# Optimization experiments

Measured on AMD Instinct MI355X. Metric: run time of the kernel, lower is better.

Reference implementation:

```python
import math
import jax, jax.numpy as jnp
import numpy as np

H = 8          # n_heads (params['h'])
TOPK_K = 2     # params['k']
TAU = 25       # moving-average window (params['tau'])


def ma_decomp(x, tau):
    """MADecompositionLayer: edge-pad by tau, centered moving average of width tau."""
    B, L, D = x.shape
    front = jnp.repeat(x[:, :1], tau, axis=1)
    back = jnp.repeat(x[:, -1:], tau, axis=1)
    padded = jnp.concatenate([front, x, back], axis=1)          # (B, L+2tau, D)
    cs = jnp.cumsum(padded, axis=1)
    cs = jnp.concatenate([jnp.zeros_like(cs[:, :1]), cs], axis=1)
    off = tau - (tau - 1) // 2  # start offset of the SAME-padded pool window
    trend = (cs[:, off + tau: off + tau + L] - cs[:, off: off + L]) / tau
    return x - trend, trend     # (seasonality, trend)


def corr_attention(x, Wq, bq, Wk, bk, Wv, bv, Wo, bo):
    """CorrLayer (inference path: per-sample top-k delay aggregation)."""
    B, L, D = x.shape
    dk = D // H
    # projections -> (B, h, d, L)
    q = (x @ Wq + bq).reshape(B, L, H, dk).transpose(0, 2, 3, 1)
    k = (x @ Wk + bk).reshape(B, L, H, dk).transpose(0, 2, 3, 1)
    v = (x @ Wv + bv).reshape(B, L, H, dk).transpose(0, 2, 3, 1)
    # FFT cross-correlation as written in the source:
    # corr = irfft(real = qr*kr, imag = -(qi*ki))
    qf = jnp.fft.rfft(q, axis=-1)
    kf = jnp.fft.rfft(k, axis=-1)
    spec = (qf.real * kf.real) - 1j * (qf.imag * kf.imag)
    corr = jnp.fft.irfft(spec, n=L, axis=-1)                    # (B, h, d, L)
    # top-k delay selection per sample
    top_k = min(int(TOPK_K * math.log(L)), L)
    mean_value = corr.mean(axis=(1, 2))                          # (B, L)
    weights, delay = jax.lax.top_k(mean_value, top_k)            # (B, topk)
    w = jax.nn.softmax(weights, axis=-1)                         # (B, topk)
    # circular-shift gather: values[..., (delay + arange(L)) % L]
    idx = (delay[:, :, None] + jnp.arange(L)[None, None, :]) % L  # (B, topk, L)
    rolled = jnp.take_along_axis(v[:, None], idx[:, :, None, None, :], axis=-1)  # (B, topk, h, d, L)
    agg = jnp.einsum('bt,bthdl->bhdl', w, rolled)                # (B, h, d, L)
    out = agg.transpose(0, 3, 1, 2).reshape(B, L, H * dk)        # (B, L, D)
    return out @ Wo + bo


def setup_inputs() -> dict:
    key = jax.random.key(0)
    ks = jax.random.split(key, 8)
    B, L, D, DFF = 8, 2048, 512, 2048
    s = 0.02
    return {
        'x':  jax.random.normal(ks[0], (B, L, D), jnp.float32),
        'Wq': jax.random.normal(ks[1], (D, D), jnp.float32) * s,
        'bq': jnp.zeros((D,), jnp.float32),
        'Wk': jax.random.normal(ks[2], (D, D), jnp.float32) * s,
        'bk': jnp.zeros((D,), jnp.float32),
        'Wv': jax.random.normal(ks[3], (D, D), jnp.float32) * s,
        'bv': jnp.zeros((D,), jnp.float32),
        'Wo': jax.random.normal(ks[4], (D, D), jnp.float32) * s,
        'bo': jnp.zeros((D,), jnp.float32),
        'W1': jax.random.normal(ks[5], (D, DFF), jnp.float32) * s,
        'W2': jax.random.normal(ks[6], (DFF, D), jnp.float32) * s,
    }


def reference(x, Wq, bq, Wk, bk, Wv, bv, Wo, bo, W1, W2):
    # Autoformer encoder layer: attn + residual, decomp, FFN, decomp
    attn_out = corr_attention(x, Wq, bq, Wk, bk, Wv, bv, Wo, bo)
    xr = x + attn_out                       # dropout_rate = 0.0
    s1, _ = ma_decomp(xr, TAU)
    y = jax.nn.relu(s1 @ W1) @ W2           # FFN (bias-free, as in Autoformer conv1d)
    s2, _ = ma_decomp(s1 + y, TAU)
    return s2
```

## Files before the change

### kernel.cpp

```cpp
#include <hip/hip_runtime.h>
#include <math.h>

namespace {
constexpr int kB = 8;
constexpr int kL = 2048;
constexpr int kD = 512;
constexpr int kTopk = 15;
constexpr int kLMask = 2047;
}

typedef unsigned short u16;
using f32x4 = __attribute__((ext_vector_type(4))) float;
using bf16x8 = __attribute__((ext_vector_type(8))) __bf16;

__device__ __forceinline__ u16 f2b(float f) {
  unsigned u = __float_as_uint(f);
  unsigned r = (u + 0x7fffu + ((u >> 16) & 1u)) >> 16;
  return (u16)r;
}
__device__ __forceinline__ float b2f(u16 u) {
  return __uint_as_float(((unsigned)u) << 16);
}

typedef __attribute__((address_space(3))) unsigned int lds_u32;
typedef __attribute__((address_space(1))) const unsigned int glb_u32;
__device__ __forceinline__ void gl2lds16(const void* g, void* l) {
  __builtin_amdgcn_global_load_lds((glb_u32*)g, (lds_u32*)l, 16, 0, 0);
}

template <int SPLIT, int RELU, int OUTF, int OUTB, int RES>
__global__ __launch_bounds__(256)
void mfma_gemm(const u16* __restrict__ A, const u16* __restrict__ Bt,
               const float* __restrict__ bias, const float* __restrict__ ResF,
               const u16* __restrict__ ResB, float* __restrict__ outF,
               u16* __restrict__ outB, int N, int K, int lda, int ldb, int nbn) {
  __shared__ u16 As[128 * 64];
  __shared__ u16 Bs[128 * 64];
  int lin = blockIdx.x;
  int split = 0;
  if (SPLIT) { split = lin >> 9; lin &= 511; }
  const int xcd = lin & 7;
  const int s = lin >> 3;
  const int q = s / nbn;
  const int bm = xcd * 16 + q;
  const int bn = s - q * nbn;
  const int tid = threadIdx.x;
  const int wave = tid >> 6;
  const int lane = tid & 63;
  const int ln = lane & 15;
  const int quad = lane >> 4;
  const int wm = (wave >> 1) * 64;
  const int wn = (wave & 1) * 64;
  const int srow = tid >> 3;
  const int scol = (tid & 7) * 8;

  const size_t koff = (size_t)split * K;
  const u16* Ab = A + koff + (size_t)(bm * 128) * lda + scol;
  const u16* Bb = Bt + koff + (size_t)(bn * 128) * ldb + scol;
  char* ldsA = (char*)As + wave * 1024;
  char* ldsB = (char*)Bs + wave * 1024;

  f32x4 acc[4][4];
#pragma unroll
  for (int i = 0; i < 4; ++i)
#pragma unroll
    for (int j = 0; j < 4; ++j) acc[i][j] = (f32x4){0.f, 0.f, 0.f, 0.f};

  for (int k0 = 0; k0 < K; k0 += 64) {
#pragma unroll
    for (int c = 0; c < 4; ++c) {
      gl2lds16(Ab + (size_t)(srow + 32 * c) * lda + k0, ldsA + c * 4096);
      gl2lds16(Bb + (size_t)(srow + 32 * c) * ldb + k0, ldsB + c * 4096);
    }
    __syncthreads();
#pragma unroll
    for (int kk = 0; kk < 2; ++kk) {
      bf16x8 af[4], bfr[4];
#pragma unroll
      for (int i = 0; i < 4; ++i)
        af[i] = *(const bf16x8*)(As + (wm + i * 16 + ln) * 64 + kk * 32 + quad * 8);
#pragma unroll
      for (int j = 0; j < 4; ++j)
        bfr[j] = *(const bf16x8*)(Bs + (wn + j * 16 + ln) * 64 + kk * 32 + quad * 8);
#pragma unroll
      for (int i = 0; i < 4; ++i)
#pragma unroll
        for (int j = 0; j < 4; ++j)
          acc[i][j] = __builtin_amdgcn_mfma_f32_16x16x32_bf16(bfr[j], af[i], acc[i][j], 0, 0, 0);
    }
    __syncthreads();
  }

  const size_t cbase = (size_t)split * ((size_t)16384 * N);
  const bool res2 = (RES == 2) && (!SPLIT || split == 0);
#pragma unroll
  for (int i = 0; i < 4; ++i) {
    const int row = bm * 128 + wm + i * 16 + ln;
#pragma unroll
    for (int j = 0; j < 4; ++j) {
      const int col = bn * 128 + wn + j * 16 + quad * 4;
      f32x4 v = acc[i][j];
      if (bias) {
        float4 bv = *(const float4*)(bias + col);
        v[0] += bv.x; v[1] += bv.y; v[2] += bv.z; v[3] += bv.w;
      }
      if (RES == 1) {
        float4 rv = *(const float4*)(ResF + (size_t)row * N + col);
        v[0] += rv.x; v[1] += rv.y; v[2] += rv.z; v[3] += rv.w;
      }
      if (RES == 2) {
        if (res2) {
          ushort4 rv = *(const ushort4*)(ResB + (size_t)row * N + col);
          v[0] += b2f(rv.x); v[1] += b2f(rv.y); v[2] += b2f(rv.z); v[3] += b2f(rv.w);
        }
      }
      if (RELU) {
#pragma unroll
        for (int r = 0; r < 4; ++r) v[r] = fmaxf(v[r], 0.f);
      }
      if (OUTF) {
        float4 o = {v[0], v[1], v[2], v[3]};
        *(float4*)(outF + cbase + (size_t)row * N + col) = o;
      }
      if (OUTB) {
        ushort4 o = {f2b(v[0]), f2b(v[1]), f2b(v[2]), f2b(v[3])};
        *(ushort4*)(outB + cbase + (size_t)row * N + col) = o;
      }
    }
  }
}

#define RDA(BUF, I, KK) \
  (*(const bf16x8*)&sm[BUF][0][arow + (I) * 1024 + ((KK) ? cx1 : cx0)])
#define RDB(BUF, J, KK) \
  (*(const bf16x8*)&sm[BUF][1][brow + (J) * 1024 + ((KK) ? cx1 : cx0)])
#define STAGE_A(BUF, Q, T) \
  gl2lds16(Ab + (size_t)(Q) * 64 * lda + (size_t)(T) * 64, \
           &sm[BUF][0][((Q) * 64 + wave * 8) * 64])
#define STAGE_B(BUF, Q, T) \
  gl2lds16(Bb + (size_t)(Q) * 64 * ldb + (size_t)(T) * 64, \
           &sm[BUF][1][((Q) * 64 + wave * 8) * 64])
#define MFMA1(i, j, kk, areg) \
  acc[i][j] = __builtin_amdgcn_mfma_f32_16x16x32_bf16(bf[j][kk], areg, acc[i][j], 0, 0, 0)
#define PHASE_MFMA(I0, A0k0, A0k1, A1k0, A1k1)                                 \
  MFMA1(I0, 0, 0, A0k0); MFMA1(I0, 1, 0, A0k0);                                \
  MFMA1(I0, 2, 0, A0k0); MFMA1(I0, 3, 0, A0k0);                                \
  MFMA1((I0) + 1, 0, 0, A1k0); MFMA1((I0) + 1, 1, 0, A1k0);                    \
  MFMA1((I0) + 1, 2, 0, A1k0); MFMA1((I0) + 1, 3, 0, A1k0);                    \
  MFMA1(I0, 0, 1, A0k1); MFMA1(I0, 1, 1, A0k1);                                \
  MFMA1(I0, 2, 1, A0k1); MFMA1(I0, 3, 1, A0k1);                                \
  MFMA1((I0) + 1, 0, 1, A1k1); MFMA1((I0) + 1, 1, 1, A1k1);                    \
  MFMA1((I0) + 1, 2, 1, A1k1); MFMA1((I0) + 1, 3, 1, A1k1)

#define GTILE(CUR, T)                                                          \
  {                                                                            \
    constexpr int NXT = (CUR) ^ 1;                                             \
    const bool hn = (T) + 1 < NT;                                              \
    const int tn = (T) + 1;                                                    \
    bf16x8 bf[4][2];                                                           \
    {                                                             \
      bf16x8 a00 = RDA(CUR, 0, 0), a01 = RDA(CUR, 0, 1);                       \
      bf16x8 a10 = RDA(CUR, 1, 0), a11 = RDA(CUR, 1, 1);                       \
      bf[0][0] = RDB(CUR, 0, 0); bf[0][1] = RDB(CUR, 0, 1);                    \
      bf[1][0] = RDB(CUR, 1, 0); bf[1][1] = RDB(CUR, 1, 1);                    \
      bf[2][0] = RDB(CUR, 2, 0); bf[2][1] = RDB(CUR, 2, 1);                    \
      bf[3][0] = RDB(CUR, 3, 0); bf[3][1] = RDB(CUR, 3, 1);                    \
      if (hn) { STAGE_B(NXT, 0, tn); STAGE_B(NXT, 1, tn); }                    \
      asm volatile("s_barrier" ::: "memory");                                  \
      __builtin_amdgcn_s_setprio(1);                                           \
      PHASE_MFMA(0, a00, a01, a10, a11);                                       \
      __builtin_amdgcn_s_setprio(0);                                           \
      asm volatile("s_barrier" ::: "memory");                                  \
    }                                                                          \
    {                                                             \
      bf16x8 a00 = RDA(CUR, 2, 0), a01 = RDA(CUR, 2, 1);                       \
      bf16x8 a10 = RDA(CUR, 3, 0), a11 = RDA(CUR, 3, 1);                       \
      if (hn) { STAGE_B(NXT, 2, tn); STAGE_B(NXT, 3, tn); }                    \
      asm volatile("s_barrier" ::: "memory");                                  \
      __builtin_amdgcn_s_setprio(1);                                           \
      PHASE_MFMA(2, a00, a01, a10, a11);                                       \
      __builtin_amdgcn_s_setprio(0);                                           \
      if (hn) { asm volatile("s_waitcnt vmcnt(4)" ::: "memory"); }             \
      else    { asm volatile("s_waitcnt vmcnt(0)" ::: "memory"); }             \
      asm volatile("s_barrier" ::: "memory");                                  \
    }                                                                          \
    {                                                             \
      bf16x8 a00 = RDA(CUR, 4, 0), a01 = RDA(CUR, 4, 1);                       \
      bf16x8 a10 = RDA(CUR, 5, 0), a11 = RDA(CUR, 5, 1);                       \
      if (hn) { STAGE_A(NXT, 0, tn); STAGE_A(NXT, 2, tn); }                    \
      asm volatile("s_barrier" ::: "memory");                                  \
      __builtin_amdgcn_s_setprio(1);                                           \
      PHASE_MFMA(4, a00, a01, a10, a11);                                       \
      __builtin_amdgcn_s_setprio(0);                                           \
      asm volatile("s_barrier" ::: "memory");                                  \
    }                                                                          \
    {                                                             \
      bf16x8 a00 = RDA(CUR, 6, 0), a01 = RDA(CUR, 6, 1);                       \
      bf16x8 a10 = RDA(CUR, 7, 0), a11 = RDA(CUR, 7, 1);                       \
      if (hn) { STAGE_A(NXT, 1, tn); STAGE_A(NXT, 3, tn); }                    \
      asm volatile("s_barrier" ::: "memory");                                  \
      __builtin_amdgcn_s_setprio(1);                                           \
      PHASE_MFMA(6, a00, a01, a10, a11);                                       \
      __builtin_amdgcn_s_setprio(0);                                           \
      if (hn) { asm volatile("s_waitcnt vmcnt(2)" ::: "memory"); }             \
      asm volatile("s_barrier" ::: "memory");                                  \
    }                                                                          \
  }

template <int SPLITK, int RELU, int HAS_BIAS, int OUTF, int RES>
__global__ __launch_bounds__(512, 2)
void gemm256(const u16* __restrict__ A, const u16* __restrict__ Bt,
             const float* __restrict__ bias, const u16* __restrict__ ResB,
             u16* __restrict__ outB, float* __restrict__ outF,
             int N, int K, int lda, int ldb, int nbn) {
  __shared__ u16 sm[2][2][256 * 64];
  const int lin = blockIdx.x;
  int bm, bn, split = 0;
  if (SPLITK) {
    const int xcd = lin & 7;
    const int s = lin >> 3;
    bm = xcd * 8 + (s & 7);
    bn = (s >> 3) & 1;
    split = s >> 4;
  } else {
    const int chunk = (int)gridDim.x >> 3;
    const int gid = (lin & 7) * chunk + (lin >> 3);
    bm = gid / nbn;
    bn = gid - bm * nbn;
  }

  const int tid = threadIdx.x;
  const int wave = tid >> 6;
  const int lane = tid & 63;
  const int ln = lane & 15;
  const int quad = lane >> 4;
  const int wm = (wave >> 2) * 128;
  const int wn = (wave & 3) * 64;

  const int srow = tid >> 3;
  const int schunk = (tid & 7) ^ (srow & 7);

  const size_t koff = (size_t)split * K;
  const u16* Ab = A + koff + (size_t)(bm * 256 + srow) * lda + schunk * 8;
  const u16* Bb = Bt + koff + (size_t)(bn * 256 + srow) * ldb + schunk * 8;

  const int cx0 = ((quad) ^ (ln & 7)) * 8;
  const int cx1 = ((4 | quad) ^ (ln & 7)) * 8;
  const int arow = (wm + ln) * 64;
  const int brow = (wn + ln) * 64;

  const int NT = K >> 6;

  f32x4 acc[8][4];
#pragma unroll
  for (int i = 0; i < 8; ++i)
#pragma unroll
    for (int j = 0; j < 4; ++j) acc[i][j] = (f32x4){0.f, 0.f, 0.f, 0.f};

  STAGE_B(0, 0, 0); STAGE_B(0, 1, 0); STAGE_B(0, 2, 0); STAGE_B(0, 3, 0);
  STAGE_A(0, 0, 0); STAGE_A(0, 2, 0); STAGE_A(0, 1, 0); STAGE_A(0, 3, 0);
  asm volatile("s_waitcnt vmcnt(2)" ::: "memory");
  asm volatile("s_barrier" ::: "memory");

  for (int t = 0; t < NT; t += 2) {
    GTILE(0, t);
    GTILE(1, t + 1);
  }

  const int col0 = bn * 256 + wn + quad * 4;
  const size_t cbase = (size_t)split * ((size_t)16384 * N);
  const int wmh = wm >> 1;

#pragma unroll
  for (int chunk = 0; chunk < 2; ++chunk) {
    if (chunk) {
      asm volatile("s_waitcnt lgkmcnt(0)" ::: "memory");
      asm volatile("s_barrier" ::: "memory");
    }
#pragma unroll
    for (int i2 = 0; i2 < 4; ++i2) {
      const int i = chunk * 4 + i2;
      const int lr = wmh + i2 * 16 + ln;
      const size_t row = (size_t)(bm * 256 + wm + i * 16 + ln);
#pragma unroll
      for (int j = 0; j < 4; ++j) {
        const int col = col0 + j * 16;
        const int ct = wn + j * 16 + quad * 4;
        f32x4 v = acc[i][j];
        if (HAS_BIAS) {
          float4 bv = *(const float4*)(bias + col);
          v[0] += bv.x; v[1] += bv.y; v[2] += bv.z; v[3] += bv.w;
        }
        if (RES == 2) {
          if (split == 0) {
            ushort4 rv = *(const ushort4*)(ResB + row * N + col);
            v[0] += b2f(rv.x); v[1] += b2f(rv.y); v[2] += b2f(rv.z); v[3] += b2f(rv.w);
          }
        }
        if (RELU) {
          v[0] = fmaxf(v[0], 0.f); v[1] = fmaxf(v[1], 0.f);
          v[2] = fmaxf(v[2], 0.f); v[3] = fmaxf(v[3], 0.f);
        }
        if (OUTF) {
          float* scrF = (float*)&sm[0][0][0];
          const int off = (lr * 1024 + ct * 4) ^ ((lr & 7) << 4);
          *(f32x4*)((char*)scrF + off) = v;
        } else {
          u16* scr = (u16*)&sm[0][0][0];
          ushort4 o = {f2b(v[0]), f2b(v[1]), f2b(v[2]), f2b(v[3])};
          const int off = (lr * 512 + ct * 2) ^ ((lr & 7) << 4);
          *(ushort4*)((char*)scr + off) = o;
        }
      }
    }
    asm volatile("s_waitcnt lgkmcnt(0)" ::: "memory");
    asm volatile("s_barrier" ::: "memory");
    if (OUTF) {
      const float* scrF = (const float*)&sm[0][0][0];
#pragma unroll
      for (int it = 0; it < 16; ++it) {
        const int idx = it * 512 + tid;
        const int r = idx >> 6;
        const int u = idx & 63;
        const int src = r * 1024 + ((u ^ (r & 7)) << 4);
        f32x4 d = *(const f32x4*)((const char*)scrF + src);
        const size_t grow = (size_t)(bm * 256 + ((r >> 6) << 7) + chunk * 64 + (r & 63));
        *((f32x4*)(outF + cbase + grow * N + bn * 256) + u) = d;
      }
    } else {
      const u16* scr = (const u16*)&sm[0][0][0];
#pragma unroll
      for (int it = 0; it < 8; ++it) {
        const int idx = it * 512 + tid;
        const int r = idx >> 5;
        const int u = idx & 31;
        const int src = r * 512 + ((u ^ (r & 7)) << 4);
        f32x4 d = *(const f32x4*)((const char*)scr + src);
        const size_t grow = (size_t)(bm * 256 + ((r >> 6) << 7) + chunk * 64 + (r & 63));
        *(f32x4*)((char*)(outB + grow * N + bn * 256) + u * 16) = d;
      }
    }
  }
}

#undef RDA
#undef RDB
#undef STAGE_A
#undef STAGE_B
#undef MFMA1
#undef PHASE_MFMA
#undef GTILE

__global__ __launch_bounds__(256)
void prep_kernel(const float* __restrict__ x,
                 const float* __restrict__ Wq, const float* __restrict__ Wk,
                 const float* __restrict__ Wv, const float* __restrict__ Wo,
                 const float* __restrict__ W1, const float* __restrict__ W2,
                 const float* __restrict__ bq, const float* __restrict__ bk,
                 const float* __restrict__ bv,
                 u16* __restrict__ xb, u16* __restrict__ Wqkvt,
                 u16* __restrict__ W1t, u16* __restrict__ W2t,
                 float* __restrict__ bqkv) {
  __shared__ float tsh[32][33];
  const int blk = blockIdx.x;
  const int tid = threadIdx.x;
  if (blk < 8192) {
    const int i = (blk * 256 + tid) * 4;
    float4 v = *(const float4*)(x + i);
    ushort4 o = {f2b(v.x), f2b(v.y), f2b(v.z), f2b(v.w)};
    *(ushort4*)(xb + i) = o;
  } else if (blk < 9216) {
    const int rem = blk - 8192;
    const int z = rem >> 8;
    const int by = (rem >> 4) & 15;
    const int bx = rem & 15;
    const float* W = z == 0 ? Wq : z == 1 ? Wk : z == 2 ? Wv : Wo;
    u16* Wt = Wqkvt + (size_t)z * 512 * 512;
    const int k0 = by * 32, n0 = bx * 32;
    const int tx = tid & 31, ty = tid >> 5;
    for (int r = ty; r < 32; r += 8)
      tsh[r][tx] = W[(size_t)(k0 + r) * 512 + n0 + tx];
    __syncthreads();
    for (int r = ty; r < 32; r += 8)
      Wt[(size_t)(n0 + r) * 512 + k0 + tx] = f2b(tsh[tx][r]);
  } else if (blk < 10240) {
    const int rem = blk - 9216;
    const int bx = rem & 63;
    const int by = rem >> 6;
    const int k0 = by * 32, n0 = bx * 32;
    const int tx = tid & 31, ty = tid >> 5;
    for (int r = ty; r < 32; r += 8)
      tsh[r][tx] = W1[(size_t)(k0 + r) * 2048 + n0 + tx];
    __syncthreads();
    for (int r = ty; r < 32; r += 8)
      W1t[(size_t)(n0 + r) * 512 + k0 + tx] = f2b(tsh[tx][r]);
  } else if (blk < 11264) {
    const int rem = blk - 10240;
    const int bx = rem & 15;
    const int by = rem >> 4;
    const int k0 = by * 32, n0 = bx * 32;
    const int tx = tid & 31, ty = tid >> 5;
    for (int r = ty; r < 32; r += 8)
      tsh[r][tx] = W2[(size_t)(k0 + r) * 512 + n0 + tx];
    __syncthreads();
    for (int r = ty; r < 32; r += 8)
      W2t[(size_t)(n0 + r) * 2048 + k0 + tx] = f2b(tsh[tx][r]);
  } else {
    const int i = (blk - 11264) * 256 + tid;
    const float* s = i < 512 ? bq : (i < 1024 ? bk : bv);
    bqkv[i] = s[i & 511];
  }
}

__global__ __launch_bounds__(256)
void fft_corr(const u16* __restrict__ qkv, float* __restrict__ pA,
              float* __restrict__ pB) {
  __shared__ u16 stq[4 * 2048];
  __shared__ u16 stk[4 * 2048];
  __shared__ float re[2048];
  __shared__ float im[2048];
  const int blk = blockIdx.x;
  const int b = blk & 7;
  const int g = blk >> 3;
  const int t = threadIdx.x;
  const float PI = 3.14159265358979323846f;

  const u16* qb = qkv + (size_t)b * kL * 1536 + g * 4;
#pragma unroll
  for (int p = 0; p < 8; ++p) {
    const int row = p * 256 + t;
    *(ushort4*)&stq[row * 4] = *(const ushort4*)(qb + (size_t)row * 1536);
    *(ushort4*)&stk[row * 4] = *(const ushort4*)(qb + (size_t)row * 1536 + 512);
  }

  const int r = t & 31;
  float cA[4], sA[4], cB[2], sB[2], cC, sC;
  float cD[4], sD[4], cE[2], sE[2], cF, sF;
#pragma unroll
  for (int j = 0; j < 4; ++j)
    __sincosf(PI * (float)(t + 256 * j) * (1.f / 1024.f), &sA[j], &cA[j]);
#pragma unroll
  for (int j = 0; j < 2; ++j)
    __sincosf(PI * (float)(t + 256 * j) * (1.f / 512.f), &sB[j], &cB[j]);
  __sincosf(PI * (float)t * (1.f / 256.f), &sC, &cC);
#pragma unroll
  for (int j = 0; j < 4; ++j)
    __sincosf(PI * (float)(r + 32 * j) * (1.f / 128.f), &sD[j], &cD[j]);
#pragma unroll
  for (int j = 0; j < 2; ++j)
    __sincosf(PI * (float)(r + 32 * j) * (1.f / 64.f), &sE[j], &cE[j]);
  __sincosf(PI * (float)r * (1.f / 32.f), &sF, &cF);
  float sgn[5], cS[5], sS[5];
#pragma unroll
  for (int k = 0; k < 5; ++k) {
    const int m = 16 >> k;
    const bool hi = (t & m) != 0;
    float sv, cv;
    __sincosf(PI * (float)(t & (m - 1)) / (float)m, &sv, &cv);
    sgn[k] = hi ? -1.f : 1.f;
    cS[k] = hi ? cv : 1.f;
    sS[k] = hi ? sv : 0.f;
  }

  float accA[8], accB[8];
#pragma unroll
  for (int i = 0; i < 8; ++i) { accA[i] = 0.f; accB[i] = 0.f; }

  const int base2 = (t >> 5) * 256 + r;

#define BFLY(X, Y, CV, SV)                                              \
  { const float dr_ = er[X] - er[Y], di_ = ei[X] - ei[Y];               \
    er[X] += er[Y]; ei[X] += ei[Y];                                     \
    er[Y] = dr_ * (CV) + di_ * (SV); ei[Y] = di_ * (CV) - dr_ * (SV); }

#pragma unroll
  for (int c = 0; c < 4; ++c) {
    __syncthreads();
    float er[8], ei[8];
#pragma unroll
    for (int j = 0; j < 8; ++j) {
      er[j] = b2f(stq[(t + 256 * j) * 4 + c]);
      ei[j] = b2f(stk[(t + 256 * j) * 4 + c]);
    }
    BFLY(0, 4, cA[0], sA[0]); BFLY(1, 5, cA[1], sA[1]);
    BFLY(2, 6, cA[2], sA[2]); BFLY(3, 7, cA[3], sA[3]);
    BFLY(0, 2, cB[0], sB[0]); BFLY(1, 3, cB[1], sB[1]);
    BFLY(4, 6, cB[0], sB[0]); BFLY(5, 7, cB[1], sB[1]);
    BFLY(0, 1, cC, sC); BFLY(2, 3, cC, sC);
    BFLY(4, 5, cC, sC); BFLY(6, 7, cC, sC);
#pragma unroll
    for (int j = 0; j < 8; ++j) {
      re[t + 256 * j] = er[j];
      im[t + 256 * j] = ei[j];
    }
    __syncthreads();
#pragma unroll
    for (int j = 0; j < 8; ++j) {
      er[j] = re[base2 + 32 * j];
      ei[j] = im[base2 + 32 * j];
    }
    BFLY(0, 4, cD[0], sD[0]); BFLY(1, 5, cD[1], sD[1]);
    BFLY(2, 6, cD[2], sD[2]); BFLY(3, 7, cD[3], sD[3]);
    BFLY(0, 2, cE[0], sE[0]); BFLY(1, 3, cE[1], sE[1]);
    BFLY(4, 6, cE[0], sE[0]); BFLY(5, 7, cE[1], sE[1]);
    BFLY(0, 1, cF, sF); BFLY(2, 3, cF, sF);
    BFLY(4, 5, cF, sF); BFLY(6, 7, cF, sF);
#pragma unroll
    for (int k = 0; k < 5; ++k) {
      const int m = 16 >> k;
#pragma unroll
      for (int j = 0; j < 8; ++j) {
        const float otr = __shfl_xor(er[j], m, 64);
        const float oti = __shfl_xor(ei[j], m, 64);
        const float sr = otr + sgn[k] * er[j];
        const float si = oti + sgn[k] * ei[j];
        er[j] = sr * cS[k] + si * sS[k];
        ei[j] = si * cS[k] - sr * sS[k];
      }
    }
    __syncthreads();
#pragma unroll
    for (int j = 0; j < 8; ++j) {
      re[base2 + 32 * j] = er[j];
      im[base2 + 32 * j] = ei[j];
    }
    __syncthreads();
#pragma unroll
    for (int i = 0; i < 8; ++i) {
      const int pos = i * 256 + t;
      const int f = __brev((unsigned)pos) >> 21;
      if (f <= 1024) {
        const int fm = (2048 - f) & 2047;
        const int pm = __brev((unsigned)fm) >> 21;
        const float zr = re[pos], zi = im[pos];
        const float mr = re[pm], mi = im[pm];
        const float ReQ = 0.5f * (zr + mr);
        const float ImQ = 0.5f * (zi - mi);
        const float ReK = 0.5f * (zi + mi);
        const float ImK = 0.5f * (mr - zr);
        accA[i] += ReQ * ReK;
        accB[i] += ImQ * ImK;
      }
    }
  }
#undef BFLY

  float* pAb = pA + (size_t)blk * 1025;
  float* pBb = pB + (size_t)blk * 1025;
#pragma unroll
  for (int i = 0; i < 8; ++i) {
    const int pos = i * 256 + t;
    const int f = __brev((unsigned)pos) >> 21;
    if (f <= 1024) { pAb[f] = accA[i]; pBb[f] = accB[i]; }
  }
}

__global__ __launch_bounds__(256)
void reduceAB(const float* __restrict__ pA, const float* __restrict__ pB,
              float* __restrict__ Asp, float* __restrict__ Bsp) {
  const int b = blockIdx.x;
  const int f = blockIdx.y * 256 + threadIdx.x;
  if (f > 1024) return;
  float sa = 0.f, sb = 0.f;
  for (int g = 0; g < 128; ++g) {
    const size_t idx = (size_t)((g << 3) | b) * 1025 + f;
    sa += pA[idx];
    sb += pB[idx];
  }
  Asp[b * 1025 + f] = sa;
  Bsp[b * 1025 + f] = sb;
}

__global__ __launch_bounds__(256)
void ifft_topk(const float* __restrict__ Asp, const float* __restrict__ Bsp,
               float* __restrict__ wts, int* __restrict__ dly) {
  __shared__ float re[2048];
  __shared__ float im[2048];
  __shared__ float twc[2047];
  __shared__ float tws[2047];
  __shared__ float rv[256];
  __shared__ int ri[256];
  __shared__ float topv[kTopk];
  __shared__ int topi[kTopk];
  const int b = blockIdx.x;
  const int t = threadIdx.x;
  for (int e = t; e < 2047; e += 256) {
    const int s = 31 - __clz(e + 1);
    const int m = 1 << s;
    const int j = e + 1 - m;
    float sv, cv;
    __sincosf((float)j * 3.14159265358979323846f / (float)m, &sv, &cv);
    twc[e] = cv;
    tws[e] = sv;
  }
#pragma unroll
  for (int i = 0; i < 8; ++i) {
    const int f = i * 256 + t;
    float Xr, Xi;
    if (f <= 1024) {
      Xr = Asp[b * 1025 + f];
      Xi = (f == 0 || f == 1024) ? 0.f : -Bsp[b * 1025 + f];
    } else {
      const int gg = 2048 - f;
      Xr = Asp[b * 1025 + gg];
      Xi = Bsp[b * 1025 + gg];
    }
    const int pos = __brev((unsigned)f) >> 21;
    re[pos] = Xr;
    im[pos] = Xi;
  }
  for (int s = 0; s <= 10; ++s) {
    __syncthreads();
    const int m = 1 << s;
    for (int p = 0; p < 4; ++p) {
      const int id = p * 256 + t;
      const int j = id & (m - 1);
      const int i0 = ((id >> s) << (s + 1)) + j;
      const int i1 = i0 + m;
      const int kk = (m - 1) + j;
      const float cv = twc[kk], sv = tws[kk];
      const float br = re[i1], bi = im[i1];
      const float tr = br * cv - bi * sv;
      const float ti = bi * cv + br * sv;
      const float ar = re[i0], ai = im[i0];
      re[i0] = ar + tr;
      im[i0] = ai + ti;
      re[i1] = ar - tr;
      im[i1] = ai - ti;
    }
  }
  __syncthreads();
#pragma unroll
  for (int i = 0; i < 8; ++i) {
    const int n = i * 256 + t;
    im[n] = re[n] * (1.0f / (2048.0f * 512.0f));
  }
  __syncthreads();
  for (int round = 0; round < kTopk; ++round) {
    float bv = -INFINITY;
    int bi = 0x7fffffff;
#pragma unroll
    for (int i = 0; i < 8; ++i) {
      const int n = i * 256 + t;
      const float v = im[n];
      if (v > bv || (v == bv && n < bi)) { bv = v; bi = n; }
    }
    rv[t] = bv;
    ri[t] = bi;
    __syncthreads();
    for (int s = 128; s > 0; s >>= 1) {
      if (t < s) {
        const float v2 = rv[t + s];
        const int i2 = ri[t + s];
        if (v2 > rv[t] || (v2 == rv[t] && i2 < ri[t])) { rv[t] = v2; ri[t] = i2; }
      }
      __syncthreads();
    }
    if (t == 0) {
      topv[round] = rv[0];
      topi[round] = ri[0];
      im[ri[0]] = -INFINITY;
    }
    __syncthreads();
  }
  if (t == 0) {
    const float m = topv[0];
    float sum = 0.f;
    float e[kTopk];
    for (int i = 0; i < kTopk; ++i) { e[i] = expf(topv[i] - m); sum += e[i]; }
    for (int i = 0; i < kTopk; ++i) {
      wts[b * 16 + i] = e[i] / sum;
      dly[b * 16 + i] = topi[i];
    }
  }
}

__global__ __launch_bounds__(256)
void agg_kernel(const u16* __restrict__ qkv, const float* __restrict__ wts,
                const int* __restrict__ dly, u16* __restrict__ out) {
  __shared__ float w[16];
  __shared__ int dl[16];
  const int lin = blockIdx.x;
  const int b = lin & 7;
  if (threadIdx.x < kTopk) {
    w[threadIdx.x] = wts[b * 16 + threadIdx.x];
    dl[threadIdx.x] = dly[b * 16 + threadIdx.x];
  }
  __syncthreads();
  const int l = (lin >> 3) * 4 + (threadIdx.x >> 6);
  const int co = (threadIdx.x & 63) * 8;
  const u16* vb = qkv + (size_t)b * kL * 1536 + 1024 + co;
  float a[8] = {0.f, 0.f, 0.f, 0.f, 0.f, 0.f, 0.f, 0.f};
  for (int t = 0; t < kTopk; ++t) {
    const int row = (l + dl[t]) & kLMask;
    float4 rv = *(const float4*)(vb + (size_t)row * 1536);
    const u16* p = (const u16*)&rv;
    const float wt = w[t];
#pragma unroll
    for (int e = 0; e < 8; ++e) a[e] += wt * b2f(p[e]);
  }
  u16 ob[8];
#pragma unroll
  for (int e = 0; e < 8; ++e) ob[e] = f2b(a[e]);
  *(float4*)(out + ((size_t)b * kL + l) * kD + co) = *(const float4*)ob;
}

__global__ __launch_bounds__(256)
void decomp_b2b(const u16* __restrict__ X, u16* __restrict__ OB) {
  const int c = blockIdx.x * 256 + threadIdx.x;
  const int b = blockIdx.y;
  const int l0 = blockIdx.z * 64;
  const u16* base = X + (size_t)b * kL * kD + c;
  float sum = 0.f;
#pragma unroll
  for (int m = -12; m <= 12; ++m) {
    int lm = l0 + m;
    lm = lm < 0 ? 0 : (lm > kL - 1 ? kL - 1 : lm);
    sum += b2f(base[(size_t)lm * kD]);
  }
#pragma unroll 4
  for (int l = l0; l < l0 + 64; ++l) {
    const float val = b2f(base[(size_t)l * kD]);
    OB[((size_t)b * kL + l) * kD + c] = f2b(val - sum * (1.0f / 25.0f));
    const int la = l + 13 > kL - 1 ? kL - 1 : l + 13;
    const int lr = l - 12 < 0 ? 0 : l - 12;
    sum += b2f(base[(size_t)la * kD]) - b2f(base[(size_t)lr * kD]);
  }
}

__global__ __launch_bounds__(256)
void decomp_ff2(const float* __restrict__ X1, const float* __restrict__ X2,
                float* __restrict__ OF) {
  const int c = blockIdx.x * 256 + threadIdx.x;
  const int b = blockIdx.y;
  const int l0 = blockIdx.z * 64;
  const size_t off = (size_t)b * kL * kD + c;
  const float* b1 = X1 + off;
  const float* b2 = X2 + off;
  float sum = 0.f;
#pragma unroll
  for (int m = -12; m <= 12; ++m) {
    int lm = l0 + m;
    lm = lm < 0 ? 0 : (lm > kL - 1 ? kL - 1 : lm);
    sum += b1[(size_t)lm * kD] + b2[(size_t)lm * kD];
  }
#pragma unroll 4
  for (int l = l0; l < l0 + 64; ++l) {
    const float val = b1[(size_t)l * kD] + b2[(size_t)l * kD];
    OF[((size_t)b * kL + l) * kD + c] = val - sum * (1.0f / 25.0f);
    const int la = l + 13 > kL - 1 ? kL - 1 : l + 13;
    const int lr = l - 12 < 0 ? 0 : l - 12;
    sum += b1[(size_t)la * kD] + b2[(size_t)la * kD]
         - b1[(size_t)lr * kD] - b2[(size_t)lr * kD];
  }
}

extern "C" void kernel_launch(void* const* d_in, const int* in_sizes, int n_in,
                              void* d_out, int out_size, void* d_ws, size_t ws_size,
                              hipStream_t stream) {
  const float* x  = (const float*)d_in[0];
  const float* Wq = (const float*)d_in[1];
  const float* bq = (const float*)d_in[2];
  const float* Wk = (const float*)d_in[3];
  const float* bk = (const float*)d_in[4];
  const float* Wv = (const float*)d_in[5];
  const float* bv = (const float*)d_in[6];
  const float* Wo = (const float*)d_in[7];
  const float* bo = (const float*)d_in[8];
  const float* W1 = (const float*)d_in[9];
  const float* W2 = (const float*)d_in[10];
  float* out = (float*)d_out;

  const size_t MiB = 1u << 20;
  const size_t NBLD = (size_t)kB * kL * kD;
  char* base = (char*)d_ws;
  u16*   qkvb  = (u16*)(base);
  u16*   xb    = (u16*)(base + 48 * MiB);
  u16*   aggb  = xb;
  u16*   xrb   = (u16*)(base + 64 * MiB);
  u16*   s1b   = (u16*)(base + 80 * MiB);
  u16*   midb  = (u16*)(base + 96 * MiB);
  float* s2p   = (float*)(base);
  u16*   Wqkvt = (u16*)(base + 160 * MiB);
  u16*   Wot   = Wqkvt + 3 * 512 * 512;
  u16*   W1t   = (u16*)(base + 162 * MiB);
  u16*   W2t   = (u16*)(base + 164 * MiB);
  float* bqkv  = (float*)(base + 166 * MiB);
  float* Asp   = bqkv + 2048;
  float* Bsp   = Asp + kB * 1025;
  float* wtsf  = Bsp + kB * 1025;
  int*   dlyi  = (int*)(wtsf + kB * 16);
  float* pA    = (float*)(base + 167 * MiB);
  float* pB    = (float*)(base + 172 * MiB);

  const dim3 blk(256);
  const dim3 blk512(512);

  prep_kernel<<<dim3(11270), blk, 0, stream>>>(
      x, Wq, Wk, Wv, Wo, W1, W2, bq, bk, bv, xb, Wqkvt, W1t, W2t, bqkv);

  gemm256<0, 0, 1, 0, 0><<<dim3(384), blk512, 0, stream>>>(
      xb, Wqkvt, bqkv, nullptr, qkvb, nullptr, 1536, 512, 512, 512, 6);

  fft_corr<<<dim3(1024), blk, 0, stream>>>(qkvb, pA, pB);
  reduceAB<<<dim3(8, 5), blk, 0, stream>>>(pA, pB, Asp, Bsp);
  ifft_topk<<<dim3(8), blk, 0, stream>>>(Asp, Bsp, wtsf, dlyi);

  agg_kernel<<<dim3(4096), blk, 0, stream>>>(qkvb, wtsf, dlyi, aggb);
  mfma_gemm<0, 0, 0, 1, 1><<<dim3(512), blk, 0, stream>>>(
      aggb, Wot, bo, x, nullptr, nullptr, xrb, 512, 512, 512, 512, 4);

  decomp_b2b<<<dim3(2, 8, 32), blk, 0, stream>>>(xrb, s1b);

  gemm256<0, 1, 0, 0, 0><<<dim3(512), blk512, 0, stream>>>(
      s1b, W1t, nullptr, nullptr, midb, nullptr, 2048, 512, 512, 512, 8);

  gemm256<1, 0, 0, 1, 2><<<dim3(256), blk512, 0, stream>>>(
      midb, W2t, nullptr, s1b, nullptr, s2p, 512, 1024, 2048, 2048, 2);

  decomp_ff2<<<dim3(2, 8, 32), blk, 0, stream>>>(s2p, s2p + NBLD, out);
}
```

Baseline: 403.5 us.

## Replace 256-tile pipelined GEMM with unified swizzled 128-tile GEMM

Removes the 256x256 double-buffered, phase-scheduled gemm256 kernel and the old mfma_gemm, replacing all four GEMMs with a single 128x128 tile kernel. The new kernel uses XOR-swizzled LDS staging and an LDS-staged coalesced epilogue, with no double buffering. Grids grow to 4x more blocks of 256 threads. This trades operand reuse and load/compute overlap for more parallelism and a simpler single-buffer loop, which risks more global traffic and exposed load latency on the larger GEMMs.

Measured after the change: 426.7 us. +5.8%, slower.

```diff
diff --git a/kernel.cpp b/kernel.cpp
--- a/kernel.cpp
+++ b/kernel.cpp
@@ -28,22 +28,25 @@
   __builtin_amdgcn_global_load_lds((glb_u32*)g, (lds_u32*)l, 16, 0, 0);
 }
 
-template <int SPLIT, int RELU, int OUTF, int OUTB, int RES>
-__global__ __launch_bounds__(256)
-void mfma_gemm(const u16* __restrict__ A, const u16* __restrict__ Bt,
-               const float* __restrict__ bias, const float* __restrict__ ResF,
-               const u16* __restrict__ ResB, float* __restrict__ outF,
-               u16* __restrict__ outB, int N, int K, int lda, int ldb, int nbn) {
-  __shared__ u16 As[128 * 64];
-  __shared__ u16 Bs[128 * 64];
+template <int SPLITK, int RELU, int HAS_BIAS, int OUTF, int RES>
+__global__ __launch_bounds__(256)
+void gemm128(const u16* __restrict__ A, const u16* __restrict__ Bt,
+             const float* __restrict__ bias, const float* __restrict__ ResF,
+             const u16* __restrict__ ResB, u16* __restrict__ outB,
+             float* __restrict__ outF, int N, int K, int lda, int ldb, int nbn) {
+  __shared__ __align__(16) u16 smu[2][128 * 64];
+  u16* As = &smu[0][0];
+  u16* Bs = &smu[1][0];
+
   int lin = blockIdx.x;
   int split = 0;
-  if (SPLIT) { split = lin >> 9; lin &= 511; }
-  const int xcd = lin & 7;
-  const int s = lin >> 3;
-  const int q = s / nbn;
-  const int bm = xcd * 16 + q;
-  const int bn = s - q * nbn;
+  const int g2 = SPLITK ? ((int)gridDim.x >> 1) : (int)gridDim.x;
+  if (SPLITK && lin >= g2) { split = 1; lin -= g2; }
+  const int chunkx = g2 >> 3;
+  const int gid = (lin & 7) * chunkx + (lin >> 3);
+  const int bm = gid / nbn;
+  const int bn = gid - bm * nbn;
+
   const int tid = threadIdx.x;
   const int wave = tid >> 6;
   const int lane = tid & 63;
@@ -51,15 +54,19 @@
   const int quad = lane >> 4;
   const int wm = (wave >> 1) * 64;
   const int wn = (wave & 1) * 64;
+
   const int srow = tid >> 3;
-  const int scol = (tid & 7) * 8;
+  const int schunk = (tid & 7) ^ (srow & 7);
 
   const size_t koff = (size_t)split * K;
-  const u16* Ab = A + koff + (size_t)(bm * 128) * lda + scol;
-  const u16* Bb = Bt + koff + (size_t)(bn * 128) * ldb + scol;
+  const u16* Ab = A + koff + (size_t)(bm * 128 + srow) * lda + schunk * 8;
+  const u16* Bb = Bt + koff + (size_t)(bn * 128 + srow) * ldb + schunk * 8;
   char* ldsA = (char*)As + wave * 1024;
   char* ldsB = (char*)Bs + wave * 1024;
 
+  const int cx0 = ((quad) ^ (ln & 7)) * 8;
+  const int cx1 = ((4 | quad) ^ (ln & 7)) * 8;
+
   f32x4 acc[4][4];
 #pragma unroll
   for (int i = 0; i < 4; ++i)
@@ -69,19 +76,20 @@
   for (int k0 = 0; k0 < K; k0 += 64) {
 #pragma unroll
     for (int c = 0; c < 4; ++c) {
-      gl2lds16(Ab + (size_t)(srow + 32 * c) * lda + k0, ldsA + c * 4096);
-      gl2lds16(Bb + (size_t)(srow + 32 * c) * ldb + k0, ldsB + c * 4096);
+      gl2lds16(Ab + (size_t)(32 * c) * lda + k0, ldsA + c * 4096);
+      gl2lds16(Bb + (size_t)(32 * c) * ldb + k0, ldsB + c * 4096);
     }
     __syncthreads();
 #pragma unroll
     for (int kk = 0; kk < 2; ++kk) {
+      const int cx = kk ? cx1 : cx0;
       bf16x8 af[4], bfr[4];
 #pragma unroll
       for (int i = 0; i < 4; ++i)
-        af[i] = *(const bf16x8*)(As + (wm + i * 16 + ln) * 64 + kk * 32 + quad * 8);
+        af[i] = *(const bf16x8*)(As + (wm + i * 16 + ln) * 64 + cx);
 #pragma unroll
       for (int j = 0; j < 4; ++j)
-        bfr[j] = *(const bf16x8*)(Bs + (wn + j * 16 + ln) * 64 + kk * 32 + quad * 8);
+        bfr[j] = *(const bf16x8*)(Bs + (wn + j * 16 + ln) * 64 + cx);
 #pragma unroll
       for (int i = 0; i < 4; ++i)
 #pragma unroll
@@ -91,197 +99,15 @@
     __syncthreads();
   }
 
+  const int col0 = bn * 128 + wn + quad * 4;
   const size_t cbase = (size_t)split * ((size_t)16384 * N);
-  const bool res2 = (RES == 2) && (!SPLIT || split == 0);
-#pragma unroll
-  for (int i = 0; i < 4; ++i) {
-    const int row = bm * 128 + wm + i * 16 + ln;
-#pragma unroll
-    for (int j = 0; j < 4; ++j) {
-      const int col = bn * 128 + wn + j * 16 + quad * 4;
-      f32x4 v = acc[i][j];
-      if (bias) {
-        float4 bv = *(const float4*)(bias + col);
-        v[0] += bv.x; v[1] += bv.y; v[2] += bv.z; v[3] += bv.w;
-      }
-      if (RES == 1) {
-        float4 rv = *(const float4*)(ResF + (size_t)row * N + col);
-        v[0] += rv.x; v[1] += rv.y; v[2] += rv.z; v[3] += rv.w;
-      }
-      if (RES == 2) {
-        if (res2) {
-          ushort4 rv = *(const ushort4*)(ResB + (size_t)row * N + col);
-          v[0] += b2f(rv.x); v[1] += b2f(rv.y); v[2] += b2f(rv.z); v[3] += b2f(rv.w);
-        }
-      }
-      if (RELU) {
-#pragma unroll
-        for (int r = 0; r < 4; ++r) v[r] = fmaxf(v[r], 0.f);
-      }
-      if (OUTF) {
-        float4 o = {v[0], v[1], v[2], v[3]};
-        *(float4*)(outF + cbase + (size_t)row * N + col) = o;
-      }
-      if (OUTB) {
-        ushort4 o = {f2b(v[0]), f2b(v[1]), f2b(v[2]), f2b(v[3])};
-        *(ushort4*)(outB + cbase + (size_t)row * N + col) = o;
-      }
-    }
-  }
-}
-
-#define RDA(BUF, I, KK) \
-  (*(const bf16x8*)&sm[BUF][0][arow + (I) * 1024 + ((KK) ? cx1 : cx0)])
-#define RDB(BUF, J, KK) \
-  (*(const bf16x8*)&sm[BUF][1][brow + (J) * 1024 + ((KK) ? cx1 : cx0)])
-#define STAGE_A(BUF, Q, T) \
-  gl2lds16(Ab + (size_t)(Q) * 64 * lda + (size_t)(T) * 64, \
-           &sm[BUF][0][((Q) * 64 + wave * 8) * 64])
-#define STAGE_B(BUF, Q, T) \
-  gl2lds16(Bb + (size_t)(Q) * 64 * ldb + (size_t)(T) * 64, \
-           &sm[BUF][1][((Q) * 64 + wave * 8) * 64])
-#define MFMA1(i, j, kk, areg) \
-  acc[i][j] = __builtin_amdgcn_mfma_f32_16x16x32_bf16(bf[j][kk], areg, acc[i][j], 0, 0, 0)
-#define PHASE_MFMA(I0, A0k0, A0k1, A1k0, A1k1)                                 \
-  MFMA1(I0, 0, 0, A0k0); MFMA1(I0, 1, 0, A0k0);                                \
-  MFMA1(I0, 2, 0, A0k0); MFMA1(I0, 3, 0, A0k0);                                \
-  MFMA1((I0) + 1, 0, 0, A1k0); MFMA1((I0) + 1, 1, 0, A1k0);                    \
-  MFMA1((I0) + 1, 2, 0, A1k0); MFMA1((I0) + 1, 3, 0, A1k0);                    \
-  MFMA1(I0, 0, 1, A0k1); MFMA1(I0, 1, 1, A0k1);                                \
-  MFMA1(I0, 2, 1, A0k1); MFMA1(I0, 3, 1, A0k1);                                \
-  MFMA1((I0) + 1, 0, 1, A1k1); MFMA1((I0) + 1, 1, 1, A1k1);                    \
-  MFMA1((I0) + 1, 2, 1, A1k1); MFMA1((I0) + 1, 3, 1, A1k1)
-
-#define GTILE(CUR, T)                                                          \
-  {                                                                            \
-    constexpr int NXT = (CUR) ^ 1;                                             \
-    const bool hn = (T) + 1 < NT;                                              \
-    const int tn = (T) + 1;                                                    \
-    bf16x8 bf[4][2];                                                           \
-    {                                                             \
-      bf16x8 a00 = RDA(CUR, 0, 0), a01 = RDA(CUR, 0, 1);                       \
-      bf16x8 a10 = RDA(CUR, 1, 0), a11 = RDA(CUR, 1, 1);                       \
-      bf[0][0] = RDB(CUR, 0, 0); bf[0][1] = RDB(CUR, 0, 1);                    \
-      bf[1][0] = RDB(CUR, 1, 0); bf[1][1] = RDB(CUR, 1, 1);                    \
-      bf[2][0] = RDB(CUR, 2, 0); bf[2][1] = RDB(CUR, 2, 1);                    \
-      bf[3][0] = RDB(CUR, 3, 0); bf[3][1] = RDB(CUR, 3, 1);                    \
-      if (hn) { STAGE_B(NXT, 0, tn); STAGE_B(NXT, 1, tn); }                    \
-      asm volatile("s_barrier" ::: "memory");                                  \
-      __builtin_amdgcn_s_setprio(1);                                           \
-      PHASE_MFMA(0, a00, a01, a10, a11);                                       \
-      __builtin_amdgcn_s_setprio(0);                                           \
-      asm volatile("s_barrier" ::: "memory");                                  \
-    }                                                                          \
-    {                                                             \
-      bf16x8 a00 = RDA(CUR, 2, 0), a01 = RDA(CUR, 2, 1);                       \
-      bf16x8 a10 = RDA(CUR, 3, 0), a11 = RDA(CUR, 3, 1);                       \
-      if (hn) { STAGE_B(NXT, 2, tn); STAGE_B(NXT, 3, tn); }                    \
-      asm volatile("s_barrier" ::: "memory");                                  \
-      __builtin_amdgcn_s_setprio(1);                                           \
-      PHASE_MFMA(2, a00, a01, a10, a11);                                       \
-      __builtin_amdgcn_s_setprio(0);                                           \
-      if (hn) { asm volatile("s_waitcnt vmcnt(4)" ::: "memory"); }             \
-      else    { asm volatile("s_waitcnt vmcnt(0)" ::: "memory"); }             \
-      asm volatile("s_barrier" ::: "memory");                                  \
-    }                                                                          \
-    {                                                             \
-      bf16x8 a00 = RDA(CUR, 4, 0), a01 = RDA(CUR, 4, 1);                       \
-      bf16x8 a10 = RDA(CUR, 5, 0), a11 = RDA(CUR, 5, 1);                       \
-      if (hn) { STAGE_A(NXT, 0, tn); STAGE_A(NXT, 2, tn); }                    \
-      asm volatile("s_barrier" ::: "memory");                                  \
-      __builtin_amdgcn_s_setprio(1);                                           \
-      PHASE_MFMA(4, a00, a01, a10, a11);                                       \
-      __builtin_amdgcn_s_setprio(0);                                           \
-      asm volatile("s_barrier" ::: "memory");                                  \
-    }                                                                          \
-    {                                                             \
-      bf16x8 a00 = RDA(CUR, 6, 0), a01 = RDA(CUR, 6, 1);                       \
-      bf16x8 a10 = RDA(CUR, 7, 0), a11 = RDA(CUR, 7, 1);                       \
-      if (hn) { STAGE_A(NXT, 1, tn); STAGE_A(NXT, 3, tn); }                    \
-      asm volatile("s_barrier" ::: "memory");                                  \
-      __builtin_amdgcn_s_setprio(1);                                           \
-      PHASE_MFMA(6, a00, a01, a10, a11);                                       \
-      __builtin_amdgcn_s_setprio(0);                                           \
-      if (hn) { asm volatile("s_waitcnt vmcnt(2)" ::: "memory"); }             \
-      asm volatile("s_barrier" ::: "memory");                                  \
-    }                                                                          \
-  }
-
-template <int SPLITK, int RELU, int HAS_BIAS, int OUTF, int RES>
-__global__ __launch_bounds__(512, 2)
-void gemm256(const u16* __restrict__ A, const u16* __restrict__ Bt,
-             const float* __restrict__ bias, const u16* __restrict__ ResB,
-             u16* __restrict__ outB, float* __restrict__ outF,
-             int N, int K, int lda, int ldb, int nbn) {
-  __shared__ u16 sm[2][2][256 * 64];
-  const int lin = blockIdx.x;
-  int bm, bn, split = 0;
-  if (SPLITK) {
-    const int xcd = lin & 7;
-    const int s = lin >> 3;
-    bm = xcd * 8 + (s & 7);
-    bn = (s >> 3) & 1;
-    split = s >> 4;
-  } else {
-    const int chunk = (int)gridDim.x >> 3;
-    const int gid = (lin & 7) * chunk + (lin >> 3);
-    bm = gid / nbn;
-    bn = gid - bm * nbn;
-  }
-
-  const int tid = threadIdx.x;
-  const int wave = tid >> 6;
-  const int lane = tid & 63;
-  const int ln = lane & 15;
-  const int quad = lane >> 4;
-  const int wm = (wave >> 2) * 128;
-  const int wn = (wave & 3) * 64;
-
-  const int srow = tid >> 3;
-  const int schunk = (tid & 7) ^ (srow & 7);
-
-  const size_t koff = (size_t)split * K;
-  const u16* Ab = A + koff + (size_t)(bm * 256 + srow) * lda + schunk * 8;
-  const u16* Bb = Bt + koff + (size_t)(bn * 256 + srow) * ldb + schunk * 8;
-
-  const int cx0 = ((quad) ^ (ln & 7)) * 8;
-  const int cx1 = ((4 | quad) ^ (ln & 7)) * 8;
-  const int arow = (wm + ln) * 64;
-  const int brow = (wn + ln) * 64;
-
-  const int NT = K >> 6;
-
-  f32x4 acc[8][4];
-#pragma unroll
-  for (int i = 0; i < 8; ++i)
-#pragma unroll
-    for (int j = 0; j < 4; ++j) acc[i][j] = (f32x4){0.f, 0.f, 0.f, 0.f};
-
-  STAGE_B(0, 0, 0); STAGE_B(0, 1, 0); STAGE_B(0, 2, 0); STAGE_B(0, 3, 0);
-  STAGE_A(0, 0, 0); STAGE_A(0, 2, 0); STAGE_A(0, 1, 0); STAGE_A(0, 3, 0);
-  asm volatile("s_waitcnt vmcnt(2)" ::: "memory");
-  asm volatile("s_barrier" ::: "memory");
-
-  for (int t = 0; t < NT; t += 2) {
-    GTILE(0, t);
-    GTILE(1, t + 1);
-  }
-
-  const int col0 = bn * 256 + wn + quad * 4;
-  const size_t cbase = (size_t)split * ((size_t)16384 * N);
-  const int wmh = wm >> 1;
-
-#pragma unroll
-  for (int chunk = 0; chunk < 2; ++chunk) {
-    if (chunk) {
-      asm volatile("s_waitcnt lgkmcnt(0)" ::: "memory");
-      asm volatile("s_barrier" ::: "memory");
-    }
-#pragma unroll
-    for (int i2 = 0; i2 < 4; ++i2) {
-      const int i = chunk * 4 + i2;
-      const int lr = wmh + i2 * 16 + ln;
-      const size_t row = (size_t)(bm * 256 + wm + i * 16 + ln);
+  u16* scr = &smu[0][0];
+
+  if (!OUTF) {
+#pragma unroll
+    for (int i = 0; i < 4; ++i) {
+      const int lr = wm + i * 16 + ln;
+      const size_t row = (size_t)(bm * 128 + lr);
 #pragma unroll
       for (int j = 0; j < 4; ++j) {
         const int col = col0 + j * 16;
@@ -291,65 +117,80 @@
           float4 bv = *(const float4*)(bias + col);
           v[0] += bv.x; v[1] += bv.y; v[2] += bv.z; v[3] += bv.w;
         }
-        if (RES == 2) {
-          if (split == 0) {
-            ushort4 rv = *(const ushort4*)(ResB + row * N + col);
-            v[0] += b2f(rv.x); v[1] += b2f(rv.y); v[2] += b2f(rv.z); v[3] += b2f(rv.w);
-          }
+        if (RES == 1) {
+          float4 rv = *(const float4*)(ResF + row * N + col);
+          v[0] += rv.x; v[1] += rv.y; v[2] += rv.z; v[3] += rv.w;
         }
         if (RELU) {
           v[0] = fmaxf(v[0], 0.f); v[1] = fmaxf(v[1], 0.f);
           v[2] = fmaxf(v[2], 0.f); v[3] = fmaxf(v[3], 0.f);
         }
-        if (OUTF) {
-          float* scrF = (float*)&sm[0][0][0];
-          const int off = (lr * 1024 + ct * 4) ^ ((lr & 7) << 4);
-          *(f32x4*)((char*)scrF + off) = v;
-        } else {
-          u16* scr = (u16*)&sm[0][0][0];
-          ushort4 o = {f2b(v[0]), f2b(v[1]), f2b(v[2]), f2b(v[3])};
-          const int off = (lr * 512 + ct * 2) ^ ((lr & 7) << 4);
-          *(ushort4*)((char*)scr + off) = o;
+        ushort4 o = {f2b(v[0]), f2b(v[1]), f2b(v[2]), f2b(v[3])};
+        const int off = (lr * 256 + ct * 2) ^ ((lr & 7) << 4);
+        *(ushort4*)((char*)scr + off) = o;
+      }
+    }
+    asm volatile("s_waitcnt lgkmcnt(0)" ::: "memory");
+    asm volatile("s_barrier" ::: "memory");
+#pragma unroll
+    for (int it = 0; it < 8; ++it) {
+      const int idx = it * 256 + tid;
+      const int r = idx >> 4;
+      const int u = idx & 15;
+      const int src = r * 256 + ((u ^ (r & 7)) << 4);
+      f32x4 d = *(const f32x4*)((const char*)scr + src);
+      *(f32x4*)((char*)(outB + (size_t)(bm * 128 + r) * N + bn * 128) + u * 16) = d;
+    }
+  } else {
+#pragma unroll
+    for (int ch = 0; ch < 2; ++ch) {
+      if (ch) {
+        asm volatile("s_waitcnt lgkmcnt(0)" ::: "memory");
+        asm volatile("s_barrier" ::: "memory");
+      }
+      if ((wm >> 6) == ch) {
+#pragma unroll
+        for (int i = 0; i < 4; ++i) {
+          const int lr2 = i * 16 + ln;
+          const size_t row = (size_t)(bm * 128 + ch * 64 + lr2);
+#pragma unroll
+          for (int j = 0; j < 4; ++j) {
+            const int col = col0 + j * 16;
+            const int ct = wn + j * 16 + quad * 4;
+            f32x4 v = acc[i][j];
+            if (HAS_BIAS) {
+              float4 bv = *(const float4*)(bias + col);
+              v[0] += bv.x; v[1] += bv.y; v[2] += bv.z; v[3] += bv.w;
+            }
+            if (RES == 2) {
+              if (split == 0) {
+                ushort4 rv = *(const ushort4*)(ResB + row * N + col);
+                v[0] += b2f(rv.x); v[1] += b2f(rv.y); v[2] += b2f(rv.z); v[3] += b2f(rv.w);
+              }
+            }
+            if (RELU) {
+              v[0] = fmaxf(v[0], 0.f); v[1] = fmaxf(v[1], 0.f);
+              v[2] = fmaxf(v[2], 0.f); v[3] = fmaxf(v[3], 0.f);
+            }
+            const int off = (lr2 * 512 + ct * 4) ^ ((lr2 & 7) << 4);
+            *(f32x4*)((char*)scr + off) = v;
+          }
         }
       }
-    }
-    asm volatile("s_waitcnt lgkmcnt(0)" ::: "memory");
-    asm volatile("s_barrier" ::: "memory");
-    if (OUTF) {
-      const float* scrF = (const float*)&sm[0][0][0];
-#pragma unroll
-      for (int it = 0; it < 16; ++it) {
-        const int idx = it * 512 + tid;
-        const int r = idx >> 6;
-        const int u = idx & 63;
-        const int src = r * 1024 + ((u ^ (r & 7)) << 4);
-        f32x4 d = *(const f32x4*)((const char*)scrF + src);
-        const size_t grow = (size_t)(bm * 256 + ((r >> 6) << 7) + chunk * 64 + (r & 63));
-        *((f32x4*)(outF + cbase + grow * N + bn * 256) + u) = d;
-      }
-    } else {
-      const u16* scr = (const u16*)&sm[0][0][0];
+      asm volatile("s_waitcnt lgkmcnt(0)" ::: "memory");
+      asm volatile("s_barrier" ::: "memory");
 #pragma unroll
       for (int it = 0; it < 8; ++it) {
-        const int idx = it * 512 + tid;
+        const int idx = it * 256 + tid;
         const int r = idx >> 5;
         const int u = idx & 31;
         const int src = r * 512 + ((u ^ (r & 7)) << 4);
         f32x4 d = *(const f32x4*)((const char*)scr + src);
-        const size_t grow = (size_t)(bm * 256 + ((r >> 6) << 7) + chunk * 64 + (r & 63));
-        *(f32x4*)((char*)(outB + grow * N + bn * 256) + u * 16) = d;
+        *(f32x4*)(outF + cbase + (size_t)(bm * 128 + ch * 64 + r) * N + bn * 128 + u * 4) = d;
       }
     }
   }
 }
-
-#undef RDA
-#undef RDB
-#undef STAGE_A
-#undef STAGE_B
-#undef MFMA1
-#undef PHASE_MFMA
-#undef GTILE
 
 __global__ __launch_bounds__(256)
 void prep_kernel(const float* __restrict__ x,
@@ -794,29 +635,28 @@
   float* pB    = (float*)(base + 172 * MiB);
 
   const dim3 blk(256);
-  const dim3 blk512(512);
 
   prep_kernel<<<dim3(11270), blk, 0, stream>>>(
       x, Wq, Wk, Wv, Wo, W1, W2, bq, bk, bv, xb, Wqkvt, W1t, W2t, bqkv);
 
-  gemm256<0, 0, 1, 0, 0><<<dim3(384), blk512, 0, stream>>>(
-      xb, Wqkvt, bqkv, nullptr, qkvb, nullptr, 1536, 512, 512, 512, 6);
+  gemm128<0, 0, 1, 0, 0><<<dim3(1536), blk, 0, stream>>>(
+      xb, Wqkvt, bqkv, nullptr, nullptr, qkvb, nullptr, 1536, 512, 512, 512, 12);
 
   fft_corr<<<dim3(1024), blk, 0, stream>>>(qkvb, pA, pB);
   reduceAB<<<dim3(8, 5), blk, 0, stream>>>(pA, pB, Asp, Bsp);
   ifft_topk<<<dim3(8), blk, 0, stream>>>(Asp, Bsp, wtsf, dlyi);
 
   agg_kernel<<<dim3(4096), blk, 0, stream>>>(qkvb, wtsf, dlyi, aggb);
-  mfma_gemm<0, 0, 0, 1, 1><<<dim3(512), blk, 0, stream>>>(
-      aggb, Wot, bo, x, nullptr, nullptr, xrb, 512, 512, 512, 512, 4);
+  gemm128<0, 0, 1, 0, 1><<<dim3(512), blk, 0, stream>>>(
+      aggb, Wot, bo, x, nullptr, xrb, nullptr, 512, 512, 512, 512, 4);
 
   decomp_b2b<<<dim3(2, 8, 32), blk, 0, stream>>>(xrb, s1b);
 
-  gemm256<0, 1, 0, 0, 0><<<dim3(512), blk512, 0, stream>>>(
-      s1b, W1t, nullptr, nullptr, midb, nullptr, 2048, 512, 512, 512, 8);
-
-  gemm256<1, 0, 0, 1, 2><<<dim3(256), blk512, 0, stream>>>(
-      midb, W2t, nullptr, s1b, nullptr, s2p, 512, 1024, 2048, 2048, 2);
+  gemm128<0, 1, 0, 0, 0><<<dim3(2048), blk, 0, stream>>>(
+      s1b, W1t, nullptr, nullptr, nullptr, midb, nullptr, 2048, 512, 512, 512, 16);
+
+  gemm128<1, 0, 0, 1, 2><<<dim3(1024), blk, 0, stream>>>(
+      midb, W2t, nullptr, nullptr, s1b, nullptr, s2p, 512, 1024, 2048, 2048, 4);
 
   decomp_ff2<<<dim3(2, 8, 32), blk, 0, stream>>>(s2p, s2p + NBLD, out);
 }
```
